# Kernel tuning notes

Measured on AMD Instinct MI355X. Metric: run time of the kernel, lower is better.

## Reference

```python
import jax, jax.numpy as jnp
import numpy as np
from jax import lax

B, C, H, W = 16, 512, 32, 32
CQ = C // 16


def _conv(x, w, b):
    # NCHW input, OIHW kernel, 3x3 stride-1 'SAME' == torch padding=1
    o = lax.conv_general_dilated(x, w, (1, 1), 'SAME',
                                 dimension_numbers=('NCHW', 'OIHW', 'NCHW'))
    return o + b[None, :, None, None]


def setup_inputs() -> dict:
    key = jax.random.key(0)
    ks = jax.random.split(key, 8)
    fan_q = C * 9
    fan_v = C * 9
    return {
        'x': jax.random.normal(ks[0], (B, C, H, W), jnp.float32),
        'y': jax.random.normal(ks[1], (B, C, H, W), jnp.float32),
        'wq': jax.random.normal(ks[2], (CQ, C, 3, 3), jnp.float32) / np.sqrt(fan_q),
        'bq': jnp.zeros((CQ,), jnp.float32),
        'wk': jax.random.normal(ks[3], (CQ, C, 3, 3), jnp.float32) / np.sqrt(fan_q),
        'bk': jnp.zeros((CQ,), jnp.float32),
        'wv': jax.random.normal(ks[4], (C, C, 3, 3), jnp.float32) / np.sqrt(fan_v),
        'bv': jnp.zeros((C,), jnp.float32),
    }


def reference(x, y, wq, bq, wk, bk, wv, bv):
    b, c, h, w = x.shape
    n = h * w
    q = _conv(x, wq, bq).reshape(b, -1, n)   # (B, CQ, N)
    k = _conv(y, wk, bk).reshape(b, -1, n)   # (B, CQ, N)
    v = _conv(y, wv, bv).reshape(b, c, n)    # (B, C, N)
    # energy[b, i, j] = <q[:, i], k[:, j]>  (unscaled, non-causal)
    energy = jnp.einsum('bdi,bdj->bij', q, k)           # (B, N, N)
    attn = jax.nn.softmax(energy, axis=-1)              # softmax over keys j
    # out[b, c, i] = sum_j v[b, c, j] * attn[b, i, j]
    out = jnp.einsum('bcj,bij->bci', v, attn)           # (B, C, N)
    return out.reshape(b, c, h, w)
```

## Files before the change

### kernel.cpp

```cpp
#include <hip/hip_runtime.h>

#define BB 16
#define CCH 512
#define CQD 32
#define HH 32
#define WW 32
#define NN 1024
#define PH 34

typedef __attribute__((ext_vector_type(8))) _Float16 half8;
typedef __attribute__((ext_vector_type(4))) _Float16 half4;
typedef __attribute__((ext_vector_type(4))) float f32x4;
typedef __attribute__((ext_vector_type(16))) float f32x16;

static __device__ __forceinline__ void gload_lds16(const void* g, void* l) {
    __builtin_amdgcn_global_load_lds(
        (const __attribute__((address_space(1))) unsigned int*)g,
        (__attribute__((address_space(3))) unsigned int*)l, 16, 0, 0);
}

__global__ __launch_bounds__(256) void prep_all_kernel(
    const float* __restrict__ x, const float* __restrict__ y,
    const float* __restrict__ wv, const float* __restrict__ wq,
    const float* __restrict__ wk,
    _Float16* __restrict__ xp, _Float16* __restrict__ yp,
    _Float16* __restrict__ wvh, _Float16* __restrict__ wqkh)
{
    const int bid = blockIdx.x;
    const int t = threadIdx.x;

    if (bid >= 1088) {
        const int wb = bid - 1088;
        const float* src;
        _Float16* dst;
        int co_src, co_dst;
        if (wb < 512)      { src = wv; co_src = wb;       dst = wvh;  co_dst = wb; }
        else if (wb < 544) { src = wq; co_src = wb - 512; dst = wqkh; co_dst = wb - 512; }
        else               { src = wk; co_src = wb - 544; dst = wqkh; co_dst = 32 + (wb - 544); }
        for (int idx = t; idx < 4608; idx += 256) {
            int tap = idx / 512, ci = idx - tap * 512;
            dst[(size_t)co_dst * 4608 + idx] = (_Float16)src[(size_t)co_src * 4608 + ci * 9 + tap];
        }
        return;
    }

    const int h = bid >> 5;
    const int which = (bid >> 4) & 1, b = bid & 15;
    const float* img = which ? y : x;
    _Float16* row = (which ? yp : xp) + (size_t)(b * PH + h) * PH * CCH;
    const int gh = h - 1;

    half8 z;
    #pragma unroll
    for (int u = 0; u < 8; ++u) z[u] = (_Float16)0.f;

    if (gh < 0 || gh >= HH) {
        for (int idx = t; idx < PH * CCH / 8; idx += 256)
            *(half8*)&row[(size_t)idx * 8] = z;
        return;
    }

    __shared__ float X[64][33];
    for (int ci0 = 0; ci0 < CCH; ci0 += 64) {
        __syncthreads();
        #pragma unroll
        for (int i = 0; i < 8; ++i) {
            int ci = i * 8 + (t >> 5), w = t & 31;
            X[ci][w] = img[((size_t)(b * CCH + ci0 + ci) * HH + gh) * WW + w];
        }
        __syncthreads();
        int w = t >> 3, g = t & 7;
        half8 o;
        #pragma unroll
        for (int u = 0; u < 8; ++u) o[u] = (_Float16)X[g * 8 + u][w];
        *(half8*)&row[(size_t)(w + 1) * CCH + ci0 + g * 8] = o;
        if (t < 16) {
            int col = (t < 8) ? 0 : 33;
            *(half8*)&row[(size_t)col * CCH + ci0 + (t & 7) * 8] = z;
        }
    }
}

__global__ __launch_bounds__(256, 2) void conv_v_mfma_kernel(
    const _Float16* __restrict__ yp,
    const _Float16* __restrict__ wvh,
    const float* __restrict__ bvb,
    _Float16* __restrict__ vout)
{
    const int pt  = blockIdx.x;
    const int co0 = blockIdx.y * 64;
    const int b   = blockIdx.z;

    __shared__ __align__(16) _Float16 Wl[64 * 296];
    __shared__ __align__(16) _Float16 Yl[13824];

    const int t    = threadIdx.x;
    const int lane = t & 63;
    const int wv4  = t >> 6;
    const int l31  = lane & 31;
    const int kh2  = lane >> 5;

    f32x16 acc[2][2];
    #pragma unroll
    for (int m = 0; m < 2; ++m)
        #pragma unroll
        for (int n = 0; n < 2; ++n)
            #pragma unroll
            for (int e = 0; e < 16; ++e) acc[m][n][e] = 0.f;

    const int r0p = pt * 8;
    int bbase[2];
    #pragma unroll
    for (int n = 0; n < 2; ++n) {
        int pxl = wv4 * 64 + n * 32 + l31;
        int rl = pxl >> 5, cl = pxl & 31;
        bbase[n] = (rl * 34 + cl) * 40 + kh2 * 8;
    }
    int abase[2];
    #pragma unroll
    for (int m = 0; m < 2; ++m)
        abase[m] = (m * 32 + l31) * 296 + kh2 * 8;

    #pragma unroll 1
    for (int ci0 = 0; ci0 < CCH; ci0 += 32) {
        __syncthreads();
        #pragma unroll
        for (int i = 0; i < 10; ++i) {
            int d = t + i * 256;
            if (d < 2368) {
                int c = d / 37, rem = d - c * 37;
                const _Float16* g = (rem < 36)
                    ? &wvh[(size_t)(co0 + c) * 4608 + (rem >> 2) * 512 + ci0 + (rem & 3) * 8]
                    : wvh;
                gload_lds16(g, (char*)Wl + (size_t)(i * 256 + wv4 * 64) * 16);
            }
        }
        #pragma unroll
        for (int i = 0; i < 7; ++i) {
            int d = t + i * 256;
            if (d < 1728) {
                int rc = d / 5, part = d - rc * 5;
                const _Float16* g = yp;
                if (rc < 340 && part < 4) {
                    int r = rc / 34, c = rc - r * 34;
                    g = &yp[((size_t)(b * PH + r0p + r) * PH + c) * CCH + ci0 + part * 8];
                }
                gload_lds16(g, (char*)Yl + (size_t)(i * 256 + wv4 * 64) * 16);
            }
        }
        __syncthreads();

        #pragma unroll
        for (int tap = 0; tap < 9; ++tap) {
            const int dh = tap / 3, dw = tap % 3;
            half8 a[2][2], bf[2][2];
            #pragma unroll
            for (int m = 0; m < 2; ++m)
                #pragma unroll
                for (int ks = 0; ks < 2; ++ks)
                    a[m][ks] = *(const half8*)&Wl[abase[m] + tap * 32 + ks * 16];
            #pragma unroll
            for (int n = 0; n < 2; ++n)
                #pragma unroll
                for (int ks = 0; ks < 2; ++ks)
                    bf[n][ks] = *(const half8*)&Yl[bbase[n] + (dh * 34 + dw) * 40 + ks * 16];
            #pragma unroll
            for (int m = 0; m < 2; ++m)
                #pragma unroll
                for (int n = 0; n < 2; ++n)
                    #pragma unroll
                    for (int ks = 0; ks < 2; ++ks)
                        acc[m][n] = __builtin_amdgcn_mfma_f32_32x32x16_f16(a[m][ks], bf[n][ks], acc[m][n], 0, 0, 0);
        }
    }

    #pragma unroll
    for (int m = 0; m < 2; ++m) {
        #pragma unroll
        for (int rq = 0; rq < 4; ++rq) {
            float4 bv = *(const float4*)&bvb[co0 + m * 32 + rq * 8 + kh2 * 4];
            #pragma unroll
            for (int e = 0; e < 4; ++e) {
                int reg = rq * 4 + e;
                int co = co0 + m * 32 + rq * 8 + kh2 * 4 + e;
                float bias = (&bv.x)[e];
                #pragma unroll
                for (int n = 0; n < 2; ++n) {
                    int px = pt * 256 + wv4 * 64 + n * 32 + l31;
                    vout[((size_t)b * CCH + co) * NN + px] = (_Float16)(acc[m][n][reg] + bias);
                }
            }
        }
    }
}

__global__ __launch_bounds__(256, 4) void conv_qk_split_kernel(
    const _Float16* __restrict__ xp,
    const _Float16* __restrict__ yp,
    const _Float16* __restrict__ wqkh,
    float* __restrict__ pbuf)
{
    const int pt    = blockIdx.x >> 2;
    const int ks    = blockIdx.x & 3;
    const int which = blockIdx.y;
    const int b     = blockIdx.z;
    const _Float16* in = which ? yp : xp;

    __shared__ __align__(16) _Float16 Wl[9728];
    __shared__ __align__(16) _Float16 Xl[8192];

    const int t    = threadIdx.x;
    const int lane = t & 63;
    const int w    = t >> 6;
    const int l15  = lane & 15;
    const int kg   = lane >> 4;

    f32x4 acc[2][2];
    #pragma unroll
    for (int m = 0; m < 2; ++m)
        #pragma unroll
        for (int n = 0; n < 2; ++n) {
            f32x4 z = {0.f, 0.f, 0.f, 0.f};
            acc[m][n] = z;
        }

    const int r0p = pt * 4;
    int bbase[2];
    #pragma unroll
    for (int n = 0; n < 2; ++n) {
        int pxl = w * 32 + n * 16 + l15;
        int rl = pxl >> 5, cl = pxl & 31;
        bbase[n] = (rl * 34 + cl) * 40 + kg * 8;
    }
    int abase[2];
    #pragma unroll
    for (int m = 0; m < 2; ++m)
        abase[m] = (m * 16 + l15) * 296 + kg * 8;

    #pragma unroll 1
    for (int cc = 0; cc < 4; ++cc) {
        const int ci0 = ks * 128 + cc * 32;
        __syncthreads();
        #pragma unroll
        for (int i = 0; i < 5; ++i) {
            int d = t + i * 256;
            if (d < 1216) {
                const _Float16* g = wqkh;
                if (d < 1184) {
                    int c = d / 37, rem = d - c * 37;
                    if (rem < 36)
                        g = &wqkh[(size_t)(which * 32 + c) * 4608 + (rem >> 2) * 512 + ci0 + (rem & 3) * 8];
                }
                gload_lds16(g, (char*)Wl + (size_t)(i * 256 + w * 64) * 16);
            }
        }
        #pragma unroll
        for (int i = 0; i < 4; ++i) {
            int d = t + i * 256;
            int rc = d / 5, part = d - rc * 5;
            const _Float16* g = in;
            if (rc < 204 && part < 4) {
                int r = rc / 34, c = rc - r * 34;
                g = &in[((size_t)(b * PH + r0p + r) * PH + c) * CCH + ci0 + part * 8];
            }
            gload_lds16(g, (char*)Xl + (size_t)(i * 256 + w * 64) * 16);
        }
        __syncthreads();

        #pragma unroll
        for (int tap = 0; tap < 9; ++tap) {
            const int dh = tap / 3, dw = tap % 3;
            half8 a[2], bfr[2];
            #pragma unroll
            for (int m = 0; m < 2; ++m)
                a[m] = *(const half8*)&Wl[abase[m] + tap * 32];
            #pragma unroll
            for (int n = 0; n < 2; ++n)
                bfr[n] = *(const half8*)&Xl[bbase[n] + (dh * 34 + dw) * 40];
            #pragma unroll
            for (int m = 0; m < 2; ++m)
                #pragma unroll
                for (int n = 0; n < 2; ++n)
                    acc[m][n] = __builtin_amdgcn_mfma_f32_16x16x32_f16(a[m], bfr[n], acc[m][n], 0, 0, 0);
        }
    }

    float* pb = &pbuf[(((size_t)(ks * 2 + which) * BB + b) * NN) * CQD];
    #pragma unroll
    for (int n = 0; n < 2; ++n) {
        int px = pt * 128 + w * 32 + n * 16 + l15;
        #pragma unroll
        for (int m = 0; m < 2; ++m) {
            float4 o = make_float4(acc[m][n][0], acc[m][n][1], acc[m][n][2], acc[m][n][3]);
            *(float4*)&pb[(size_t)px * CQD + m * 16 + kg * 4] = o;
        }
    }
}

__global__ __launch_bounds__(256) void qk_reduce_kernel(
    const float* __restrict__ pbuf,
    const float* __restrict__ bq, const float* __restrict__ bk,
    _Float16* __restrict__ qh, _Float16* __restrict__ kh)
{
    const int gid   = blockIdx.x * 256 + threadIdx.x;
    const int cog   = gid & 7;
    const int px    = (gid >> 3) & 1023;
    const int b     = (gid >> 13) & 15;
    const int which = gid >> 17;

    const size_t base = (((size_t)which * BB + b) * NN + px) * CQD + cog * 4;
    const size_t kstep = (size_t)2 * BB * NN * CQD;
    float4 s = *(const float4*)&pbuf[base];
    #pragma unroll
    for (int ks = 1; ks < 4; ++ks) {
        float4 p = *(const float4*)&pbuf[base + ks * kstep];
        s.x += p.x; s.y += p.y; s.z += p.z; s.w += p.w;
    }
    const float* bias = which ? bk : bq;
    float4 bv = *(const float4*)&bias[cog * 4];
    half4 o;
    o[0] = (_Float16)(s.x + bv.x);
    o[1] = (_Float16)(s.y + bv.y);
    o[2] = (_Float16)(s.z + bv.z);
    o[3] = (_Float16)(s.w + bv.w);
    _Float16* out = which ? kh : qh;
    *(half4*)&out[((size_t)b * NN + px) * CQD + cog * 4] = o;
}

__global__ __launch_bounds__(256, 2) void attn_fused_kernel(
    const _Float16* __restrict__ qh,
    const _Float16* __restrict__ kh,
    const _Float16* __restrict__ v,
    float* __restrict__ out)
{
    const int wg   = blockIdx.x;
    const int virt = (wg & 7) * 64 + (wg >> 3);
    const int b    = virt >> 5;
    const int i0   = (virt & 31) * 32;

    __shared__ __align__(16) _Float16 Vl[2][128 * 136];
    __shared__ __align__(16) _Float16 Pl[32 * 136];
    float* redm = (float*)Pl;
    float* redl = redm + 32 * 17;

    const int t    = threadIdx.x;
    const int lane = t & 63;
    const int w    = t >> 6;
    const int l15  = lane & 15;
    const int kg   = lane >> 4;

    #define STAGE_V(dst, jp_, cc_)                                              \
        {                                                                       \
            _Pragma("unroll")                                                   \
            for (int i_ = 0; i_ < 9; ++i_) {                                    \
                int d_ = t + i_ * 256;                                          \
                if (d_ < 2176) {                  \
                    int r_ = d_ / 17, rem_ = d_ - r_ * 17;                      \
                    const _Float16* g_ = (rem_ < 16)                            \
                        ? &v[((size_t)b * CCH + (cc_) * 128 + r_) * NN + (jp_) * 128 + rem_ * 8] \
                        : v;                                                    \
                    gload_lds16(g_, (char*)(dst) + (size_t)(i_ * 256 + w * 64) * 16); \
                }                                                               \
            }                                                                   \
        }

    half8 qb[2];
    #pragma unroll
    for (int n = 0; n < 2; ++n)
        qb[n] = *(const half8*)&qh[((size_t)b * NN + i0 + n * 16 + l15) * CQD + kg * 8];

    float m[2] = {-3.0e38f, -3.0e38f}, l[2] = {0.f, 0.f};
    #pragma unroll 1
    for (int jp = 0; jp < 8; ++jp) {
        #pragma unroll
        for (int ht = 0; ht < 2; ++ht) {
            int j = jp * 128 + ht * 64 + w * 16 + l15;
            half8 ak = *(const half8*)&kh[((size_t)b * NN + j) * CQD + kg * 8];
            #pragma unroll
            for (int n = 0; n < 2; ++n) {
                f32x4 s = {0.f, 0.f, 0.f, 0.f};
                s = __builtin_amdgcn_mfma_f32_16x16x32_f16(ak, qb[n], s, 0, 0, 0);
                float tm = fmaxf(fmaxf(s[0], s[1]), fmaxf(s[2], s[3]));
                float m2 = fmaxf(m[n], tm);
                l[n] = l[n] * __expf(m[n] - m2)
                     + __expf(s[0] - m2) + __expf(s[1] - m2)
                     + __expf(s[2] - m2) + __expf(s[3] - m2);
                m[n] = m2;
            }
        }
    }
    #pragma unroll
    for (int n = 0; n < 2; ++n) {
        redm[(n * 16 + l15) * 17 + w * 4 + kg] = m[n];
        redl[(n * 16 + l15) * 17 + w * 4 + kg] = l[n];
    }
    __syncthreads();
    float mr[2], rl[2];
    #pragma unroll
    for (int n = 0; n < 2; ++n) {
        const int i = n * 16 + l15;
        float M = redm[i * 17];
        #pragma unroll
        for (int p = 1; p < 16; ++p) M = fmaxf(M, redm[i * 17 + p]);
        float L = 0.f;
        #pragma unroll
        for (int p = 0; p < 16; ++p) L += redl[i * 17 + p] * __expf(redm[i * 17 + p] - M);
        mr[n] = M;
        rl[n] = 1.f / L;
    }

    f32x4 acc[4][2][2];
    #pragma unroll
    for (int cc = 0; cc < 4; ++cc)
        #pragma unroll
        for (int mm = 0; mm < 2; ++mm)
            #pragma unroll
            for (int n = 0; n < 2; ++n) {
                f32x4 z = {0.f, 0.f, 0.f, 0.f};
                acc[cc][mm][n] = z;
            }

    #pragma unroll 1
    for (int jp = 0; jp < 8; ++jp) {
        __syncthreads();
        STAGE_V(Vl[0], jp, 0);
        #pragma unroll
        for (int ht = 0; ht < 2; ++ht) {
            int j = jp * 128 + ht * 64 + w * 16 + l15;
            half8 ak = *(const half8*)&kh[((size_t)b * NN + j) * CQD + kg * 8];
            #pragma unroll
            for (int n = 0; n < 2; ++n) {
                f32x4 s = {0.f, 0.f, 0.f, 0.f};
                s = __builtin_amdgcn_mfma_f32_16x16x32_f16(ak, qb[n], s, 0, 0, 0);
                half4 p4;
                #pragma unroll
                for (int reg = 0; reg < 4; ++reg)
                    p4[reg] = (_Float16)(__expf(s[reg] - mr[n]) * rl[n]);
                *(half4*)&Pl[(n * 16 + l15) * 136 + ht * 64 + w * 16 + kg * 4] = p4;
            }
        }
        #pragma unroll
        for (int cc = 0; cc < 4; ++cc) {
            __syncthreads();
            if (cc < 3) {
                _Float16* vnxt = (_Float16*)Vl[(cc + 1) & 1];
                STAGE_V(vnxt, jp, cc + 1);
            }
            const _Float16* vcur = (const _Float16*)Vl[cc & 1];
            #pragma unroll
            for (int ks = 0; ks < 4; ++ks) {
                half8 pb[2], va[2];
                #pragma unroll
                for (int n = 0; n < 2; ++n)
                    pb[n] = *(const half8*)&Pl[(n * 16 + l15) * 136 + ks * 32 + kg * 8];
                #pragma unroll
                for (int mm = 0; mm < 2; ++mm)
                    va[mm] = *(const half8*)&vcur[(w * 32 + mm * 16 + l15) * 136 + ks * 32 + kg * 8];
                #pragma unroll
                for (int mm = 0; mm < 2; ++mm)
                    #pragma unroll
                    for (int n = 0; n < 2; ++n)
                        acc[cc][mm][n] = __builtin_amdgcn_mfma_f32_16x16x32_f16(va[mm], pb[n], acc[cc][mm][n], 0, 0, 0);
            }
        }
    }

    #pragma unroll
    for (int cc = 0; cc < 4; ++cc)
        #pragma unroll
        for (int mm = 0; mm < 2; ++mm)
            #pragma unroll
            for (int n = 0; n < 2; ++n)
                #pragma unroll
                for (int reg = 0; reg < 4; ++reg) {
                    int c = cc * 128 + w * 32 + mm * 16 + kg * 4 + reg;
                    out[((size_t)b * CCH + c) * NN + i0 + n * 16 + l15] = acc[cc][mm][n][reg];
                }
    #undef STAGE_V
}

extern "C" void kernel_launch(void* const* d_in, const int* in_sizes, int n_in,
                              void* d_out, int out_size, void* d_ws, size_t ws_size,
                              hipStream_t stream) {
    const float* x  = (const float*)d_in[0];
    const float* y  = (const float*)d_in[1];
    const float* wq = (const float*)d_in[2];
    const float* bq = (const float*)d_in[3];
    const float* wk = (const float*)d_in[4];
    const float* bk = (const float*)d_in[5];
    const float* wv = (const float*)d_in[6];
    const float* bv = (const float*)d_in[7];
    float* out = (float*)d_out;

    _Float16* qhb = (_Float16*)d_ws;
    _Float16* khb = qhb + (size_t)BB * NN * CQD;
    _Float16* vb   = khb + (size_t)BB * NN * CQD;
    _Float16* ypb  = vb + (size_t)BB * CCH * NN;
    _Float16* xpb  = ypb + (size_t)BB * PH * PH * CCH;
    _Float16* wvh  = xpb + (size_t)BB * PH * PH * CCH;
    _Float16* wqkh = wvh + (size_t)512 * 4608;
    float* pbuf = (float*)vb;

    prep_all_kernel<<<dim3(1088 + 576), 256, 0, stream>>>(x, y, wv, wq, wk, xpb, ypb, wvh, wqkh);
    conv_qk_split_kernel<<<dim3(32, 2, BB), 256, 0, stream>>>(xpb, ypb, wqkh, pbuf);
    qk_reduce_kernel<<<dim3(1024), 256, 0, stream>>>(pbuf, bq, bk, qhb, khb);
    conv_v_mfma_kernel<<<dim3(4, 8, BB), 256, 0, stream>>>(ypb, wvh, bv, vb);
    attn_fused_kernel<<<dim3(512), 256, 0, stream>>>(qhb, khb, vb, out);
}
```

Measured before the change: 175.5 us.

## Double-buffer LDS staging in value convolution to overlap loads with MFMA

Splits the weight and input LDS tiles of the value convolution kernel into two buffers. The next channel chunk is loaded asynchronously into one buffer while MFMAs run on the other, which removes the second barrier per iteration. Doubling LDS use forces the launch bound down from two blocks per CU to one, so latency hiding now relies on software prefetch instead of co-resident blocks.

```diff
diff --git a/kernel.cpp b/kernel.cpp
--- a/kernel.cpp
+++ b/kernel.cpp
@@ -81,7 +81,7 @@
     }
 }
 
-__global__ __launch_bounds__(256, 2) void conv_v_mfma_kernel(
+__global__ __launch_bounds__(256, 1) void conv_v_mfma_kernel(
     const _Float16* __restrict__ yp,
     const _Float16* __restrict__ wvh,
     const float* __restrict__ bvb,
@@ -91,8 +91,8 @@
     const int co0 = blockIdx.y * 64;
     const int b   = blockIdx.z;
 
-    __shared__ __align__(16) _Float16 Wl[64 * 296];
-    __shared__ __align__(16) _Float16 Yl[13824];
+    __shared__ __align__(16) _Float16 Wl[2][64 * 296];
+    __shared__ __align__(16) _Float16 Yl[2][13824];
 
     const int t    = threadIdx.x;
     const int lane = t & 63;
@@ -121,34 +121,49 @@
     for (int m = 0; m < 2; ++m)
         abase[m] = (m * 32 + l31) * 296 + kh2 * 8;
 
+    #define STAGE_W(buf, ci0_)                                                  \
+        {                                                                       \
+            _Pragma("unroll")                                                   \
+            for (int i_ = 0; i_ < 10; ++i_) {                                   \
+                int d_ = t + i_ * 256;                                          \
+                if (d_ < 2368) {                  \
+                    int c_ = d_ / 37, rem_ = d_ - c_ * 37;                      \
+                    const _Float16* g_ = (rem_ < 36)                            \
+                        ? &wvh[(size_t)(co0 + c_) * 4608 + (rem_ >> 2) * 512 + (ci0_) + (rem_ & 3) * 8] \
+                        : wvh;                                                  \
+                    gload_lds16(g_, (char*)(buf) + (size_t)(i_ * 256 + wv4 * 64) * 16); \
+                }                                                               \
+            }                                                                   \
+        }
+    #define STAGE_Y(buf, ci0_)                                                  \
+        {                                                                       \
+            _Pragma("unroll")                                                   \
+            for (int i_ = 0; i_ < 7; ++i_) {                                    \
+                int d_ = t + i_ * 256;                                          \
+                if (d_ < 1728) {                  \
+                    int rc_ = d_ / 5, part_ = d_ - rc_ * 5;                     \
+                    const _Float16* g_ = yp;                                    \
+                    if (rc_ < 340 && part_ < 4) {                               \
+                        int r_ = rc_ / 34, c_ = rc_ - r_ * 34;                  \
+                        g_ = &yp[((size_t)(b * PH + r0p + r_) * PH + c_) * CCH + (ci0_) + part_ * 8]; \
+                    }                                                           \
+                    gload_lds16(g_, (char*)(buf) + (size_t)(i_ * 256 + wv4 * 64) * 16); \
+                }                                                               \
+            }                                                                   \
+        }
+
+    STAGE_W(Wl[0], 0);
+    STAGE_Y(Yl[0], 0);
+
     #pragma unroll 1
-    for (int ci0 = 0; ci0 < CCH; ci0 += 32) {
+    for (int s = 0; s < 16; ++s) {
         __syncthreads();
-        #pragma unroll
-        for (int i = 0; i < 10; ++i) {
-            int d = t + i * 256;
-            if (d < 2368) {
-                int c = d / 37, rem = d - c * 37;
-                const _Float16* g = (rem < 36)
-                    ? &wvh[(size_t)(co0 + c) * 4608 + (rem >> 2) * 512 + ci0 + (rem & 3) * 8]
-                    : wvh;
-                gload_lds16(g, (char*)Wl + (size_t)(i * 256 + wv4 * 64) * 16);
-            }
-        }
-        #pragma unroll
-        for (int i = 0; i < 7; ++i) {
-            int d = t + i * 256;
-            if (d < 1728) {
-                int rc = d / 5, part = d - rc * 5;
-                const _Float16* g = yp;
-                if (rc < 340 && part < 4) {
-                    int r = rc / 34, c = rc - r * 34;
-                    g = &yp[((size_t)(b * PH + r0p + r) * PH + c) * CCH + ci0 + part * 8];
-                }
-                gload_lds16(g, (char*)Yl + (size_t)(i * 256 + wv4 * 64) * 16);
-            }
-        }
-        __syncthreads();
+        if (s < 15) {
+            STAGE_W(Wl[(s + 1) & 1], (s + 1) * 32);
+            STAGE_Y(Yl[(s + 1) & 1], (s + 1) * 32);
+        }
+        const _Float16* Wc = Wl[s & 1];
+        const _Float16* Yc = Yl[s & 1];
 
         #pragma unroll
         for (int tap = 0; tap < 9; ++tap) {
@@ -158,12 +173,12 @@
             for (int m = 0; m < 2; ++m)
                 #pragma unroll
                 for (int ks = 0; ks < 2; ++ks)
-                    a[m][ks] = *(const half8*)&Wl[abase[m] + tap * 32 + ks * 16];
+                    a[m][ks] = *(const half8*)&Wc[abase[m] + tap * 32 + ks * 16];
             #pragma unroll
             for (int n = 0; n < 2; ++n)
                 #pragma unroll
                 for (int ks = 0; ks < 2; ++ks)
-                    bf[n][ks] = *(const half8*)&Yl[bbase[n] + (dh * 34 + dw) * 40 + ks * 16];
+                    bf[n][ks] = *(const half8*)&Yc[bbase[n] + (dh * 34 + dw) * 40 + ks * 16];
             #pragma unroll
             for (int m = 0; m < 2; ++m)
                 #pragma unroll
@@ -192,6 +207,8 @@
             }
         }
     }
+    #undef STAGE_W
+    #undef STAGE_Y
 }
 
 __global__ __launch_bounds__(256, 4) void conv_qk_split_kernel(
```

New measurement: 188.5 us, median of 2. 7.4% more time.
